# Performance work log

Measured on AMD Instinct MI355X. Metric: run time of the kernel, lower is better.

## Reference

```python
import jax, jax.numpy as jnp
import numpy as np
from jax import lax

B, T, F = 4096, 100, 40
H_ENC, H_LAT, H_DEC = 64, 32, 64


def _lstm(x, Wih, Whh, b):
    """PyTorch-convention LSTM (gate order i,f,g,o), batch_first, zero init state.
    x: [B,T,Fin], Wih: [4H,Fin], Whh: [4H,H], b: [4H] (= b_ih + b_hh).
    Returns hidden sequence [B,T,H]."""
    H = Whh.shape[1]
    # precompute input contributions for all timesteps in one GEMM
    xg = jnp.einsum('btf,gf->btg', x, Wih) + b  # [B,T,4H]
    h0 = jnp.zeros((x.shape[0], H), dtype=x.dtype)
    c0 = jnp.zeros((x.shape[0], H), dtype=x.dtype)

    def step(carry, gx_t):
        h, c = carry
        gates = gx_t + h @ Whh.T  # [B,4H]
        i, f, g, o = jnp.split(gates, 4, axis=-1)
        c = jax.nn.sigmoid(f) * c + jax.nn.sigmoid(i) * jnp.tanh(g)
        h = jax.nn.sigmoid(o) * jnp.tanh(c)
        return (h, c), h

    _, hs = lax.scan(step, (h0, c0), jnp.swapaxes(xg, 0, 1))  # [T,B,H]
    return jnp.swapaxes(hs, 0, 1)


def setup_inputs() -> dict:
    key = jax.random.key(0)
    ks = jax.random.split(key, 8)
    s = 0.05
    return {
        'x': jax.random.normal(ks[0], (B, T, F), dtype=jnp.float32),
        'enc_Wih': jax.random.normal(ks[1], (4 * H_ENC, F), dtype=jnp.float32) * s,
        'enc_Whh': jax.random.normal(ks[2], (4 * H_ENC, H_ENC), dtype=jnp.float32) * s,
        'enc_b': jnp.zeros((4 * H_ENC,), dtype=jnp.float32),
        'lat_Wih': jax.random.normal(ks[3], (4 * H_LAT, H_ENC), dtype=jnp.float32) * s,
        'lat_Whh': jax.random.normal(ks[4], (4 * H_LAT, H_LAT), dtype=jnp.float32) * s,
        'lat_b': jnp.zeros((4 * H_LAT,), dtype=jnp.float32),
        'dec_Wih': jax.random.normal(ks[5], (4 * H_DEC, H_LAT), dtype=jnp.float32) * s,
        'dec_Whh': jax.random.normal(ks[6], (4 * H_DEC, H_DEC), dtype=jnp.float32) * s,
        'dec_b': jnp.zeros((4 * H_DEC,), dtype=jnp.float32),
        'out_W': jax.random.normal(ks[7], (F, H_DEC), dtype=jnp.float32) * s,
        'out_b': jnp.zeros((F,), dtype=jnp.float32),
    }


def reference(x, enc_Wih, enc_Whh, enc_b, lat_Wih, lat_Whh, lat_b,
              dec_Wih, dec_Whh, dec_b, out_W, out_b):
    h = _lstm(x, enc_Wih, enc_Whh, enc_b)                 # [B,T,64]
    last = h[:, -1:, :]                                   # [B,1,64]
    rep = jnp.broadcast_to(last, (h.shape[0], h.shape[1], last.shape[-1]))
    h = _lstm(rep, lat_Wih, lat_Whh, lat_b)               # [B,T,32]
    h = _lstm(h, dec_Wih, dec_Whh, dec_b)                 # [B,T,64]
    return jnp.einsum('bth,fh->btf', h, out_W) + out_b    # [B,T,40]
```

## Files before the change

### kernel.cpp

```cpp
#include <hip/hip_runtime.h>
#include <cstddef>

typedef __attribute__((ext_vector_type(8))) short bf16x8;
typedef __attribute__((ext_vector_type(4))) float f32x4;

#define MFMA(a, b, c) __builtin_amdgcn_mfma_f32_16x16x32_bf16((a), (b), (c), 0, 0, 0)

static __device__ __forceinline__ unsigned short f2bf(float f) {
  unsigned u = __builtin_bit_cast(unsigned, f);
  u = u + 0x7FFFu + ((u >> 16) & 1u);
  return (unsigned short)(u >> 16);
}
static __device__ __forceinline__ float bf2f(unsigned short h) {
  unsigned u = ((unsigned)h) << 16;
  return __builtin_bit_cast(float, u);
}
static __device__ __forceinline__ float fast_sig(float x) {
  return __builtin_amdgcn_rcpf(1.0f + __expf(-x));
}
static __device__ __forceinline__ float fast_tanh(float x) {
  return 2.0f * __builtin_amdgcn_rcpf(1.0f + __expf(-2.0f * x)) - 1.0f;
}

static __device__ __forceinline__ void lds_barrier() {
  asm volatile("s_waitcnt lgkmcnt(0)\n\ts_barrier" ::: "memory");
}

static __device__ __forceinline__ bf16x8 aread(const char* base, int lane, int kc) {
  int b = lane & 15, g = lane >> 4;
  int off = (kc * 64 + g * 16) ^ ((b & 7) << 4);
  return *(const bf16x8*)(base + b * 256 + off);
}
static __device__ __forceinline__ void awrite16(char* base, int b, int k, unsigned short v) {
  int off = (2 * k) ^ ((b & 7) << 4);
  *(unsigned short*)(base + b * 256 + off) = v;
}
static __device__ __forceinline__ void awrite32(char* base, int b, int k, unsigned v) {
  int off = (2 * k) ^ ((b & 7) << 4);
  *(unsigned*)(base + b * 256 + off) = v;
}

extern "C" __global__ __launch_bounds__(512, 2)
void lstm_ae_mfma5(const float* __restrict__ x,
                   const float* __restrict__ eWih, const float* __restrict__ eWhh, const float* __restrict__ eb,
                   const float* __restrict__ lWih, const float* __restrict__ lWhh, const float* __restrict__ lb,
                   const float* __restrict__ dWih, const float* __restrict__ dWhh, const float* __restrict__ db,
                   const float* __restrict__ oW,  const float* __restrict__ ob,
                   float* __restrict__ out)
{
  __shared__ __align__(16) char sAhi[2][4096];
  __shared__ __align__(16) char sAlo[2][4096];

  const int tid  = threadIdx.x;
  const int lane = tid & 63;
  const int w    = tid >> 6;
  const int c16  = lane & 15;
  const int p4   = lane >> 4;
  const int bbase = blockIdx.x * 16;

  {
    f32x4 z = {0.f, 0.f, 0.f, 0.f};
    *(f32x4*)(&sAhi[0][0] + tid * 16) = z;
    *(f32x4*)(&sAlo[0][0] + tid * 16) = z;
  }

  bf16x8 ewh[2][4], ewl[2][4];
  float ebias[2][4];
#pragma unroll
  for (int n = 0; n < 2; ++n) {
    int tr = c16;
    int u = w * 8 + (tr >> 2) * 2 + n;
    int ga = tr & 3;
#pragma unroll
    for (int r = 0; r < 4; ++r) ebias[n][r] = eb[r * 64 + (w * 8 + p4 * 2 + n)];
#pragma unroll
    for (int kc = 0; kc < 4; ++kc) {
      bf16x8 hi, lo;
#pragma unroll
      for (int e = 0; e < 8; ++e) {
        int k = kc * 32 + p4 * 8 + e;
        float v = 0.f;
        if (k < 40)       v = eWih[(ga * 64 + u) * 40 + k];
        else if (k >= 64) v = eWhh[(ga * 64 + u) * 64 + (k - 64)];
        unsigned short hh = f2bf(v);
        hi[e] = (short)hh;
        lo[e] = (short)f2bf(v - bf2f(hh));
      }
      ewh[n][kc] = hi; ewl[n][kc] = lo;
    }
  }

  lds_barrier();

  const bool stager = (tid < 160);
  const int sb = tid / 10, sf4 = tid - (tid / 10) * 10;
  if (stager) {
    f32x4 ld = *(const f32x4*)(x + ((size_t)(bbase + sb) * 100 + 0) * 40 + sf4 * 4);
    unsigned long long ph = 0, pl = 0;
#pragma unroll
    for (int e = 0; e < 4; ++e) {
      unsigned short hh = f2bf(ld[e]);
      unsigned short ll = f2bf(ld[e] - bf2f(hh));
      ph |= (unsigned long long)hh << (16 * e);
      pl |= (unsigned long long)ll << (16 * e);
    }
    int off = (sf4 * 8) ^ ((sb & 7) << 4);
    *(unsigned long long*)(sAhi[0] + sb * 256 + off) = ph;
    *(unsigned long long*)(sAlo[0] + sb * 256 + off) = pl;
  }
  f32x4 xldA = {0.f, 0.f, 0.f, 0.f}, xldB = {0.f, 0.f, 0.f, 0.f};
  if (stager)
    xldA = *(const f32x4*)(x + ((size_t)(bbase + sb) * 100 + 1) * 40 + sf4 * 4);

  float cE[2] = {0.f, 0.f};
  lds_barrier();

  auto enc_step = [&](int t, const char* Rh, const char* Rl, char* Wh, char* Wl,
                      f32x4& xin, f32x4& xout) {
    if (stager) {
      unsigned long long ph = 0, pl = 0;
#pragma unroll
      for (int e = 0; e < 4; ++e) {
        unsigned short hh = f2bf(xin[e]);
        unsigned short ll = f2bf(xin[e] - bf2f(hh));
        ph |= (unsigned long long)hh << (16 * e);
        pl |= (unsigned long long)ll << (16 * e);
      }
      int off = (sf4 * 8) ^ ((sb & 7) << 4);
      *(unsigned long long*)(Wh + sb * 256 + off) = ph;
      *(unsigned long long*)(Wl + sb * 256 + off) = pl;
      int tn = (t + 2 <= 99) ? t + 2 : 99;
      xout = *(const f32x4*)(x + ((size_t)(bbase + sb) * 100 + tn) * 40 + sf4 * 4);
    }

    f32x4 acc[2], acc2[2];
#pragma unroll
    for (int n = 0; n < 2; ++n) {
      acc[n]  = f32x4{ebias[n][0], ebias[n][1], ebias[n][2], ebias[n][3]};
      acc2[n] = f32x4{0.f, 0.f, 0.f, 0.f};
    }
#pragma unroll
    for (int kc = 0; kc < 4; ++kc) {
      bf16x8 ah = aread(Rh, lane, kc);
      bf16x8 al = aread(Rl, lane, kc);
#pragma unroll
      for (int n = 0; n < 2; ++n) {
        f32x4 t0 = (kc < 2) ? acc[n] : acc2[n];
        t0 = MFMA(ewh[n][kc], ah, t0);
        t0 = MFMA(ewl[n][kc], ah, t0);
        t0 = MFMA(ewh[n][kc], al, t0);
        if (kc < 2) acc[n] = t0; else acc2[n] = t0;
      }
    }

    unsigned short hh[2], hl[2];
#pragma unroll
    for (int n = 0; n < 2; ++n) {
      f32x4 gv = acc[n] + acc2[n];
      float ii = fast_sig(gv[0]), ff = fast_sig(gv[1]);
      float gg = fast_tanh(gv[2]), oo = fast_sig(gv[3]);
      cE[n] = ff * cE[n] + ii * gg;
      float hv = oo * fast_tanh(cE[n]);
      hh[n] = f2bf(hv);
      hl[n] = f2bf(hv - bf2f(hh[n]));
    }
    awrite32(Wh, c16, 64 + w * 8 + p4 * 2, (unsigned)hh[0] | ((unsigned)hh[1] << 16));
    awrite32(Wl, c16, 64 + w * 8 + p4 * 2, (unsigned)hl[0] | ((unsigned)hl[1] << 16));

    lds_barrier();
  };

#pragma unroll 1
  for (int tt = 0; tt < 100; tt += 2) {
    enc_step(tt,     sAhi[0], sAlo[0], sAhi[1], sAlo[1], xldA, xldB);
    enc_step(tt + 1, sAhi[1], sAlo[1], sAhi[0], sAlo[0], xldB, xldA);
  }

  f32x4 xga;
  {
    int tr = c16;
    int u = w * 4 + (tr >> 2), ga = tr & 3;
    int ul = w * 4 + p4;
    xga = f32x4{lb[ul], lb[32 + ul], lb[64 + ul], lb[96 + ul]};
#pragma unroll
    for (int kci = 0; kci < 2; ++kci) {
      bf16x8 hi, lo;
#pragma unroll
      for (int e = 0; e < 8; ++e) {
        float v = lWih[(ga * 32 + u) * 64 + kci * 32 + p4 * 8 + e];
        unsigned short hh = f2bf(v);
        hi[e] = (short)hh;
        lo[e] = (short)f2bf(v - bf2f(hh));
      }
      bf16x8 ah = aread(sAhi[0], lane, 2 + kci);
      bf16x8 al = aread(sAlo[0], lane, 2 + kci);
      xga = MFMA(hi, ah, xga);
      xga = MFMA(lo, ah, xga);
      xga = MFMA(hi, al, xga);
    }
  }
  lds_barrier();

  {
    f32x4 z = {0.f, 0.f, 0.f, 0.f};
    *(f32x4*)(&sAhi[0][0] + tid * 16) = z;
    *(f32x4*)(&sAlo[0][0] + tid * 16) = z;
  }

  bf16x8 lwh, lwl;
  {
    int tr = c16;
    int u = w * 4 + (tr >> 2), ga = tr & 3;
    bf16x8 hi, lo;
#pragma unroll
    for (int e = 0; e < 8; ++e) {
      float v = lWhh[(ga * 32 + u) * 32 + p4 * 8 + e];
      unsigned short hh = f2bf(v);
      hi[e] = (short)hh;
      lo[e] = (short)f2bf(v - bf2f(hh));
    }
    lwh = hi; lwl = lo;
  }
  bf16x8 dwh[2][3], dwl[2][3];
  float dbias[2][4];
#pragma unroll
  for (int n = 0; n < 2; ++n) {
    int tr = c16;
    int u = w * 8 + (tr >> 2) * 2 + n;
    int ga = tr & 3;
#pragma unroll
    for (int r = 0; r < 4; ++r) dbias[n][r] = db[r * 64 + (w * 8 + p4 * 2 + n)];
#pragma unroll
    for (int kc = 0; kc < 3; ++kc) {
      bf16x8 hi, lo;
#pragma unroll
      for (int e = 0; e < 8; ++e) {
        int k = kc * 32 + p4 * 8 + e;
        float v = (k < 32) ? dWih[(ga * 64 + u) * 32 + k]
                           : dWhh[(ga * 64 + u) * 64 + (k - 32)];
        unsigned short hh = f2bf(v);
        hi[e] = (short)hh;
        lo[e] = (short)f2bf(v - bf2f(hh));
      }
      dwh[n][kc] = hi; dwl[n][kc] = lo;
    }
  }
  bf16x8 pwh[2], pwl[2];
  float pbias[4];
#pragma unroll
  for (int r = 0; r < 4; ++r) {
    int f = w * 16 + p4 * 4 + r;
    pbias[r] = (w < 3 && f < 40) ? ob[f] : 0.0f;
  }
  if (w < 3) {
    int f = w * 16 + c16;
#pragma unroll
    for (int kci = 0; kci < 2; ++kci) {
      bf16x8 hi, lo;
#pragma unroll
      for (int e = 0; e < 8; ++e) {
        float v = (f < 40) ? oW[f * 64 + kci * 32 + p4 * 8 + e] : 0.0f;
        unsigned short hh = f2bf(v);
        hi[e] = (short)hh;
        lo[e] = (short)f2bf(v - bf2f(hh));
      }
      pwh[kci] = hi; pwl[kci] = lo;
    }
  }

  float cL = 0.f;
  float cD[2] = {0.f, 0.f};
  lds_barrier();

#pragma unroll 1
  for (int i = 0; i < 102; ++i) {
    const int pa = i & 1;
    bf16x8 c0h = aread(sAhi[pa ^ 1], lane, 0), c0l = aread(sAlo[pa ^ 1], lane, 0);
    bf16x8 d1h = aread(sAhi[pa], lane, 1),     d1l = aread(sAlo[pa], lane, 1);
    bf16x8 d2h = aread(sAhi[pa], lane, 2),     d2l = aread(sAlo[pa], lane, 2);

    if (i < 100) {
      f32x4 lac = xga;
      lac = MFMA(lwh, c0h, lac);
      lac = MFMA(lwl, c0h, lac);
      lac = MFMA(lwh, c0l, lac);
      float ii = fast_sig(lac[0]), ff = fast_sig(lac[1]);
      float gg = fast_tanh(lac[2]), oo = fast_sig(lac[3]);
      cL = ff * cL + ii * gg;
      float hv = oo * fast_tanh(cL);
      unsigned short hhh = f2bf(hv);
      awrite16(sAhi[pa], c16, w * 4 + p4, hhh);
      awrite16(sAlo[pa], c16, w * 4 + p4, f2bf(hv - bf2f(hhh)));
    }

    if (i >= 1 && i < 101) {
      unsigned short hh[2], hl[2];
#pragma unroll
      for (int n = 0; n < 2; ++n) {
        f32x4 dac = f32x4{dbias[n][0], dbias[n][1], dbias[n][2], dbias[n][3]};
        dac = MFMA(dwh[n][0], c0h, dac);
        dac = MFMA(dwl[n][0], c0h, dac);
        dac = MFMA(dwh[n][0], c0l, dac);
        dac = MFMA(dwh[n][1], d1h, dac);
        dac = MFMA(dwl[n][1], d1h, dac);
        dac = MFMA(dwh[n][1], d1l, dac);
        dac = MFMA(dwh[n][2], d2h, dac);
        dac = MFMA(dwl[n][2], d2h, dac);
        dac = MFMA(dwh[n][2], d2l, dac);
        float ii = fast_sig(dac[0]), ff = fast_sig(dac[1]);
        float gg = fast_tanh(dac[2]), oo = fast_sig(dac[3]);
        cD[n] = ff * cD[n] + ii * gg;
        float hv = oo * fast_tanh(cD[n]);
        hh[n] = f2bf(hv);
        hl[n] = f2bf(hv - bf2f(hh[n]));
      }
      awrite32(sAhi[pa ^ 1], c16, 32 + w * 8 + p4 * 2, (unsigned)hh[0] | ((unsigned)hh[1] << 16));
      awrite32(sAlo[pa ^ 1], c16, 32 + w * 8 + p4 * 2, (unsigned)hl[0] | ((unsigned)hl[1] << 16));
    }

    if (i >= 2 && w < 3) {
      f32x4 pac = f32x4{pbias[0], pbias[1], pbias[2], pbias[3]};
      pac = MFMA(pwh[0], d1h, pac);
      pac = MFMA(pwl[0], d1h, pac);
      pac = MFMA(pwh[0], d1l, pac);
      pac = MFMA(pwh[1], d2h, pac);
      pac = MFMA(pwl[1], d2h, pac);
      pac = MFMA(pwh[1], d2l, pac);
#pragma unroll
      for (int r = 0; r < 4; ++r) {
        int f = w * 16 + p4 * 4 + r;
        if (f < 40)
          out[((size_t)(bbase + c16) * 100 + (i - 2)) * 40 + f] = pac[r];
      }
    }
    lds_barrier();
  }
}

extern "C" void kernel_launch(void* const* d_in, const int* in_sizes, int n_in,
                              void* d_out, int out_size, void* d_ws, size_t ws_size,
                              hipStream_t stream) {
  const float* x    = (const float*)d_in[0];
  const float* eWih = (const float*)d_in[1];
  const float* eWhh = (const float*)d_in[2];
  const float* eb   = (const float*)d_in[3];
  const float* lWih = (const float*)d_in[4];
  const float* lWhh = (const float*)d_in[5];
  const float* lb   = (const float*)d_in[6];
  const float* dWih = (const float*)d_in[7];
  const float* dWhh = (const float*)d_in[8];
  const float* db   = (const float*)d_in[9];
  const float* oW   = (const float*)d_in[10];
  const float* ob   = (const float*)d_in[11];
  float* out = (float*)d_out;

  lstm_ae_mfma5<<<256, 512, 0, stream>>>(x, eWih, eWhh, eb, lWih, lWhh, lb,
                                         dWih, dWhh, db, oW, ob, out);
}
```

Before: 184.1 us.

## Split LSTM work across 16 waves with producer/consumer encoder input projection

Doubles the block to 1024 threads. In the encoder, 8 waves compute the input projection for the next timestep and hand the partial gates to the other 8 waves through a new LDS buffer. Those 8 recurrent waves add only the hidden-state contribution, which shortens each wave's per-step MFMA chain. The decoder is re-split so each of 16 waves handles one gate unit column, the latent LSTM runs on 8 waves, and the output projection moves to waves 13-15. Occupancy drops to one block per CU and LDS use grows, in exchange for shorter serial dependency chains per step.

```diff
diff --git a/kernel.cpp b/kernel.cpp
--- a/kernel.cpp
+++ b/kernel.cpp
@@ -40,8 +40,8 @@
   *(unsigned*)(base + b * 256 + off) = v;
 }
 
-extern "C" __global__ __launch_bounds__(512, 2)
-void lstm_ae_mfma5(const float* __restrict__ x,
+extern "C" __global__ __launch_bounds__(1024, 1)
+void lstm_ae_mfma6(const float* __restrict__ x,
                    const float* __restrict__ eWih, const float* __restrict__ eWhh, const float* __restrict__ eb,
                    const float* __restrict__ lWih, const float* __restrict__ lWhh, const float* __restrict__ lb,
                    const float* __restrict__ dWih, const float* __restrict__ dWhh, const float* __restrict__ db,
@@ -50,6 +50,7 @@
 {
   __shared__ __align__(16) char sAhi[2][4096];
   __shared__ __align__(16) char sAlo[2][4096];
+  __shared__ __align__(16) char sP[2][16384];
 
   const int tid  = threadIdx.x;
   const int lane = tid & 63;
@@ -57,129 +58,145 @@
   const int c16  = lane & 15;
   const int p4   = lane >> 4;
   const int bbase = blockIdx.x * 16;
-
-  {
+  const bool xw = (w < 8);
+  const int p   = w & 7;
+
+  if (tid < 512) {
     f32x4 z = {0.f, 0.f, 0.f, 0.f};
     *(f32x4*)(&sAhi[0][0] + tid * 16) = z;
     *(f32x4*)(&sAlo[0][0] + tid * 16) = z;
   }
 
-  bf16x8 ewh[2][4], ewl[2][4];
+  bf16x8 wfh[2][2], wfl[2][2];
   float ebias[2][4];
 #pragma unroll
   for (int n = 0; n < 2; ++n) {
-    int tr = c16;
-    int u = w * 8 + (tr >> 2) * 2 + n;
-    int ga = tr & 3;
-#pragma unroll
-    for (int r = 0; r < 4; ++r) ebias[n][r] = eb[r * 64 + (w * 8 + p4 * 2 + n)];
-#pragma unroll
-    for (int kc = 0; kc < 4; ++kc) {
+    int u = p * 8 + (c16 >> 2) * 2 + n;
+    int ga = c16 & 3;
+    if (xw) {
+#pragma unroll
+      for (int r = 0; r < 4; ++r) ebias[n][r] = eb[r * 64 + (p * 8 + p4 * 2 + n)];
+    }
+#pragma unroll
+    for (int kci = 0; kci < 2; ++kci) {
       bf16x8 hi, lo;
 #pragma unroll
       for (int e = 0; e < 8; ++e) {
-        int k = kc * 32 + p4 * 8 + e;
-        float v = 0.f;
-        if (k < 40)       v = eWih[(ga * 64 + u) * 40 + k];
-        else if (k >= 64) v = eWhh[(ga * 64 + u) * 64 + (k - 64)];
+        int k = kci * 32 + p4 * 8 + e;
+        float v;
+        if (xw) v = (k < 40) ? eWih[(ga * 64 + u) * 40 + k] : 0.0f;
+        else    v = eWhh[(ga * 64 + u) * 64 + k];
         unsigned short hh = f2bf(v);
         hi[e] = (short)hh;
         lo[e] = (short)f2bf(v - bf2f(hh));
       }
-      ewh[n][kc] = hi; ewl[n][kc] = lo;
-    }
-  }
-
-  lds_barrier();
-
-  const bool stager = (tid < 160);
-  const int sb = tid / 10, sf4 = tid - (tid / 10) * 10;
-  if (stager) {
-    f32x4 ld = *(const f32x4*)(x + ((size_t)(bbase + sb) * 100 + 0) * 40 + sf4 * 4);
-    unsigned long long ph = 0, pl = 0;
-#pragma unroll
-    for (int e = 0; e < 4; ++e) {
-      unsigned short hh = f2bf(ld[e]);
-      unsigned short ll = f2bf(ld[e] - bf2f(hh));
-      ph |= (unsigned long long)hh << (16 * e);
-      pl |= (unsigned long long)ll << (16 * e);
-    }
-    int off = (sf4 * 8) ^ ((sb & 7) << 4);
-    *(unsigned long long*)(sAhi[0] + sb * 256 + off) = ph;
-    *(unsigned long long*)(sAlo[0] + sb * 256 + off) = pl;
-  }
-  f32x4 xldA = {0.f, 0.f, 0.f, 0.f}, xldB = {0.f, 0.f, 0.f, 0.f};
-  if (stager)
-    xldA = *(const f32x4*)(x + ((size_t)(bbase + sb) * 100 + 1) * 40 + sf4 * 4);
+      wfh[n][kci] = hi; wfl[n][kci] = lo;
+    }
+  }
+
+  lds_barrier();
+
+  const bool st = (tid < 320);
+  const int sbb = tid / 20, sf0 = (tid % 20) * 2;
+  if (st) {
+#pragma unroll
+    for (int tau = 0; tau < 2; ++tau) {
+      float2 v = *(const float2*)(x + ((size_t)(bbase + sbb) * 100 + tau) * 40 + sf0);
+      unsigned short h0 = f2bf(v.x), h1 = f2bf(v.y);
+      unsigned short l0 = f2bf(v.x - bf2f(h0)), l1 = f2bf(v.y - bf2f(h1));
+      awrite32(sAhi[tau], sbb, sf0, (unsigned)h0 | ((unsigned)h1 << 16));
+      awrite32(sAlo[tau], sbb, sf0, (unsigned)l0 | ((unsigned)l1 << 16));
+    }
+  }
+  float2 xin = {0.f, 0.f};
+  if (st) xin = *(const float2*)(x + ((size_t)(bbase + sbb) * 100 + 2) * 40 + sf0);
+  lds_barrier();
+
+  const int pswz  = (c16 & 7) << 4;
+  const int poff0 = (c16 * 1024 + (p * 32 + p4 * 4) * 4) ^ pswz;
+  const int poff1 = (c16 * 1024 + (p * 32 + 16 + p4 * 4) * 4) ^ pswz;
+
+  if (xw) {
+    bf16x8 x0h = aread(sAhi[0], lane, 0), x0l = aread(sAlo[0], lane, 0);
+    bf16x8 x1h = aread(sAhi[0], lane, 1), x1l = aread(sAlo[0], lane, 1);
+#pragma unroll
+    for (int n = 0; n < 2; ++n) {
+      f32x4 aA = f32x4{ebias[n][0], ebias[n][1], ebias[n][2], ebias[n][3]};
+      aA = MFMA(wfh[n][0], x0h, aA);
+      aA = MFMA(wfl[n][0], x0h, aA);
+      aA = MFMA(wfh[n][0], x0l, aA);
+      f32x4 aB = f32x4{0.f, 0.f, 0.f, 0.f};
+      aB = MFMA(wfh[n][1], x1h, aB);
+      aB = MFMA(wfl[n][1], x1h, aB);
+      aB = MFMA(wfh[n][1], x1l, aB);
+      f32x4 r = aA + aB;
+      *(f32x4*)(sP[0] + ((n == 0) ? poff0 : poff1)) = r;
+    }
+  }
+  lds_barrier();
 
   float cE[2] = {0.f, 0.f};
-  lds_barrier();
-
-  auto enc_step = [&](int t, const char* Rh, const char* Rl, char* Wh, char* Wl,
-                      f32x4& xin, f32x4& xout) {
-    if (stager) {
-      unsigned long long ph = 0, pl = 0;
-#pragma unroll
-      for (int e = 0; e < 4; ++e) {
-        unsigned short hh = f2bf(xin[e]);
-        unsigned short ll = f2bf(xin[e] - bf2f(hh));
-        ph |= (unsigned long long)hh << (16 * e);
-        pl |= (unsigned long long)ll << (16 * e);
-      }
-      int off = (sf4 * 8) ^ ((sb & 7) << 4);
-      *(unsigned long long*)(Wh + sb * 256 + off) = ph;
-      *(unsigned long long*)(Wl + sb * 256 + off) = pl;
-      int tn = (t + 2 <= 99) ? t + 2 : 99;
-      xout = *(const f32x4*)(x + ((size_t)(bbase + sb) * 100 + tn) * 40 + sf4 * 4);
-    }
-
-    f32x4 acc[2], acc2[2];
-#pragma unroll
-    for (int n = 0; n < 2; ++n) {
-      acc[n]  = f32x4{ebias[n][0], ebias[n][1], ebias[n][2], ebias[n][3]};
-      acc2[n] = f32x4{0.f, 0.f, 0.f, 0.f};
-    }
-#pragma unroll
-    for (int kc = 0; kc < 4; ++kc) {
-      bf16x8 ah = aread(Rh, lane, kc);
-      bf16x8 al = aread(Rl, lane, kc);
+
+#pragma unroll 1
+  for (int t = 0; t < 100; ++t) {
+    const int rb = (t + 1) & 1, wb = t & 1;
+    if (xw) {
+      bf16x8 x0h = aread(sAhi[rb], lane, 0), x0l = aread(sAlo[rb], lane, 0);
+      bf16x8 x1h = aread(sAhi[rb], lane, 1), x1l = aread(sAlo[rb], lane, 1);
 #pragma unroll
       for (int n = 0; n < 2; ++n) {
-        f32x4 t0 = (kc < 2) ? acc[n] : acc2[n];
-        t0 = MFMA(ewh[n][kc], ah, t0);
-        t0 = MFMA(ewl[n][kc], ah, t0);
-        t0 = MFMA(ewh[n][kc], al, t0);
-        if (kc < 2) acc[n] = t0; else acc2[n] = t0;
-      }
-    }
-
-    unsigned short hh[2], hl[2];
-#pragma unroll
-    for (int n = 0; n < 2; ++n) {
-      f32x4 gv = acc[n] + acc2[n];
-      float ii = fast_sig(gv[0]), ff = fast_sig(gv[1]);
-      float gg = fast_tanh(gv[2]), oo = fast_sig(gv[3]);
-      cE[n] = ff * cE[n] + ii * gg;
-      float hv = oo * fast_tanh(cE[n]);
-      hh[n] = f2bf(hv);
-      hl[n] = f2bf(hv - bf2f(hh[n]));
-    }
-    awrite32(Wh, c16, 64 + w * 8 + p4 * 2, (unsigned)hh[0] | ((unsigned)hh[1] << 16));
-    awrite32(Wl, c16, 64 + w * 8 + p4 * 2, (unsigned)hl[0] | ((unsigned)hl[1] << 16));
-
+        f32x4 aA = f32x4{ebias[n][0], ebias[n][1], ebias[n][2], ebias[n][3]};
+        aA = MFMA(wfh[n][0], x0h, aA);
+        aA = MFMA(wfl[n][0], x0h, aA);
+        aA = MFMA(wfh[n][0], x0l, aA);
+        f32x4 aB = f32x4{0.f, 0.f, 0.f, 0.f};
+        aB = MFMA(wfh[n][1], x1h, aB);
+        aB = MFMA(wfl[n][1], x1h, aB);
+        aB = MFMA(wfh[n][1], x1l, aB);
+        f32x4 r = aA + aB;
+        *(f32x4*)(sP[rb] + ((n == 0) ? poff0 : poff1)) = r;
+      }
+      if (st) {
+        unsigned short h0 = f2bf(xin.x), h1 = f2bf(xin.y);
+        unsigned short l0 = f2bf(xin.x - bf2f(h0)), l1 = f2bf(xin.y - bf2f(h1));
+        awrite32(sAhi[wb], sbb, sf0, (unsigned)h0 | ((unsigned)h1 << 16));
+        awrite32(sAlo[wb], sbb, sf0, (unsigned)l0 | ((unsigned)l1 << 16));
+        int tn = (t + 3 <= 99) ? t + 3 : 99;
+        xin = *(const float2*)(x + ((size_t)(bbase + sbb) * 100 + tn) * 40 + sf0);
+      }
+    } else {
+      f32x4 acc0 = *(const f32x4*)(sP[wb] + poff0);
+      f32x4 acc1 = *(const f32x4*)(sP[wb] + poff1);
+      bf16x8 h2h = aread(sAhi[rb], lane, 2), h2l = aread(sAlo[rb], lane, 2);
+      bf16x8 h3h = aread(sAhi[rb], lane, 3), h3l = aread(sAlo[rb], lane, 3);
+      unsigned short hh[2], hl[2];
+#pragma unroll
+      for (int n = 0; n < 2; ++n) {
+        f32x4 aA = (n == 0) ? acc0 : acc1;
+        aA = MFMA(wfh[n][0], h2h, aA);
+        aA = MFMA(wfl[n][0], h2h, aA);
+        aA = MFMA(wfh[n][0], h2l, aA);
+        f32x4 aB = f32x4{0.f, 0.f, 0.f, 0.f};
+        aB = MFMA(wfh[n][1], h3h, aB);
+        aB = MFMA(wfl[n][1], h3h, aB);
+        aB = MFMA(wfh[n][1], h3l, aB);
+        f32x4 gv = aA + aB;
+        float ii = fast_sig(gv[0]), ff = fast_sig(gv[1]);
+        float gg = fast_tanh(gv[2]), oo = fast_sig(gv[3]);
+        cE[n] = ff * cE[n] + ii * gg;
+        float hv = oo * fast_tanh(cE[n]);
+        hh[n] = f2bf(hv);
+        hl[n] = f2bf(hv - bf2f(hh[n]));
+      }
+      awrite32(sAhi[wb], c16, 64 + p * 8 + p4 * 2, (unsigned)hh[0] | ((unsigned)hh[1] << 16));
+      awrite32(sAlo[wb], c16, 64 + p * 8 + p4 * 2, (unsigned)hl[0] | ((unsigned)hl[1] << 16));
+    }
     lds_barrier();
-  };
-
-#pragma unroll 1
-  for (int tt = 0; tt < 100; tt += 2) {
-    enc_step(tt,     sAhi[0], sAlo[0], sAhi[1], sAlo[1], xldA, xldB);
-    enc_step(tt + 1, sAhi[1], sAlo[1], sAhi[0], sAlo[0], xldB, xldA);
-  }
-
-  f32x4 xga;
-  {
-    int tr = c16;
-    int u = w * 4 + (tr >> 2), ga = tr & 3;
+  }
+
+  f32x4 xga = {0.f, 0.f, 0.f, 0.f};
+  if (w < 8) {
+    int u = w * 4 + (c16 >> 2), ga = c16 & 3;
     int ul = w * 4 + p4;
     xga = f32x4{lb[ul], lb[32 + ul], lb[64 + ul], lb[96 + ul]};
 #pragma unroll
@@ -192,8 +209,8 @@
         hi[e] = (short)hh;
         lo[e] = (short)f2bf(v - bf2f(hh));
       }
-      bf16x8 ah = aread(sAhi[0], lane, 2 + kci);
-      bf16x8 al = aread(sAlo[0], lane, 2 + kci);
+      bf16x8 ah = aread(sAhi[1], lane, 2 + kci);
+      bf16x8 al = aread(sAlo[1], lane, 2 + kci);
       xga = MFMA(hi, ah, xga);
       xga = MFMA(lo, ah, xga);
       xga = MFMA(hi, al, xga);
@@ -201,35 +218,20 @@
   }
   lds_barrier();
 
-  {
+  if (tid < 512) {
     f32x4 z = {0.f, 0.f, 0.f, 0.f};
     *(f32x4*)(&sAhi[0][0] + tid * 16) = z;
     *(f32x4*)(&sAlo[0][0] + tid * 16) = z;
   }
 
-  bf16x8 lwh, lwl;
+  bf16x8 dwh[3], dwl[3];
+  float dbias[4];
   {
-    int tr = c16;
-    int u = w * 4 + (tr >> 2), ga = tr & 3;
-    bf16x8 hi, lo;
-#pragma unroll
-    for (int e = 0; e < 8; ++e) {
-      float v = lWhh[(ga * 32 + u) * 32 + p4 * 8 + e];
-      unsigned short hh = f2bf(v);
-      hi[e] = (short)hh;
-      lo[e] = (short)f2bf(v - bf2f(hh));
-    }
-    lwh = hi; lwl = lo;
-  }
-  bf16x8 dwh[2][3], dwl[2][3];
-  float dbias[2][4];
-#pragma unroll
-  for (int n = 0; n < 2; ++n) {
-    int tr = c16;
-    int u = w * 8 + (tr >> 2) * 2 + n;
-    int ga = tr & 3;
-#pragma unroll
-    for (int r = 0; r < 4; ++r) dbias[n][r] = db[r * 64 + (w * 8 + p4 * 2 + n)];
+    int u = (w >> 1) * 8 + (c16 >> 2) * 2 + (w & 1);
+    int ga = c16 & 3;
+    int un = (w >> 1) * 8 + p4 * 2 + (w & 1);
+#pragma unroll
+    for (int r = 0; r < 4; ++r) dbias[r] = db[r * 64 + un];
 #pragma unroll
     for (int kc = 0; kc < 3; ++kc) {
       bf16x8 hi, lo;
@@ -242,18 +244,32 @@
         hi[e] = (short)hh;
         lo[e] = (short)f2bf(v - bf2f(hh));
       }
-      dwh[n][kc] = hi; dwl[n][kc] = lo;
-    }
-  }
-  bf16x8 pwh[2], pwl[2];
+      dwh[kc] = hi; dwl[kc] = lo;
+    }
+  }
+  bf16x8 lwh = {}, lwl = {};
+  if (w < 8) {
+    int u = w * 4 + (c16 >> 2), ga = c16 & 3;
+    bf16x8 hi, lo;
+#pragma unroll
+    for (int e = 0; e < 8; ++e) {
+      float v = lWhh[(ga * 32 + u) * 32 + p4 * 8 + e];
+      unsigned short hh = f2bf(v);
+      hi[e] = (short)hh;
+      lo[e] = (short)f2bf(v - bf2f(hh));
+    }
+    lwh = hi; lwl = lo;
+  }
+  bf16x8 pwh[2] = {}, pwl[2] = {};
   float pbias[4];
+  const int wp = w - 13;
 #pragma unroll
   for (int r = 0; r < 4; ++r) {
-    int f = w * 16 + p4 * 4 + r;
-    pbias[r] = (w < 3 && f < 40) ? ob[f] : 0.0f;
-  }
-  if (w < 3) {
-    int f = w * 16 + c16;
+    int f = wp * 16 + p4 * 4 + r;
+    pbias[r] = (w >= 13 && f < 40) ? ob[f] : 0.0f;
+  }
+  if (w >= 13) {
+    int f = wp * 16 + c16;
 #pragma unroll
     for (int kci = 0; kci < 2; ++kci) {
       bf16x8 hi, lo;
@@ -268,8 +284,7 @@
     }
   }
 
-  float cL = 0.f;
-  float cD[2] = {0.f, 0.f};
+  float cL = 0.f, cD = 0.f;
   lds_barrier();
 
 #pragma unroll 1
@@ -279,7 +294,7 @@
     bf16x8 d1h = aread(sAhi[pa], lane, 1),     d1l = aread(sAlo[pa], lane, 1);
     bf16x8 d2h = aread(sAhi[pa], lane, 2),     d2l = aread(sAlo[pa], lane, 2);
 
-    if (i < 100) {
+    if (i < 100 && w < 8) {
       f32x4 lac = xga;
       lac = MFMA(lwh, c0h, lac);
       lac = MFMA(lwl, c0h, lac);
@@ -294,41 +309,42 @@
     }
 
     if (i >= 1 && i < 101) {
-      unsigned short hh[2], hl[2];
-#pragma unroll
-      for (int n = 0; n < 2; ++n) {
-        f32x4 dac = f32x4{dbias[n][0], dbias[n][1], dbias[n][2], dbias[n][3]};
-        dac = MFMA(dwh[n][0], c0h, dac);
-        dac = MFMA(dwl[n][0], c0h, dac);
-        dac = MFMA(dwh[n][0], c0l, dac);
-        dac = MFMA(dwh[n][1], d1h, dac);
-        dac = MFMA(dwl[n][1], d1h, dac);
-        dac = MFMA(dwh[n][1], d1l, dac);
-        dac = MFMA(dwh[n][2], d2h, dac);
-        dac = MFMA(dwl[n][2], d2h, dac);
-        dac = MFMA(dwh[n][2], d2l, dac);
-        float ii = fast_sig(dac[0]), ff = fast_sig(dac[1]);
-        float gg = fast_tanh(dac[2]), oo = fast_sig(dac[3]);
-        cD[n] = ff * cD[n] + ii * gg;
-        float hv = oo * fast_tanh(cD[n]);
-        hh[n] = f2bf(hv);
-        hl[n] = f2bf(hv - bf2f(hh[n]));
-      }
-      awrite32(sAhi[pa ^ 1], c16, 32 + w * 8 + p4 * 2, (unsigned)hh[0] | ((unsigned)hh[1] << 16));
-      awrite32(sAlo[pa ^ 1], c16, 32 + w * 8 + p4 * 2, (unsigned)hl[0] | ((unsigned)hl[1] << 16));
-    }
-
-    if (i >= 2 && w < 3) {
-      f32x4 pac = f32x4{pbias[0], pbias[1], pbias[2], pbias[3]};
-      pac = MFMA(pwh[0], d1h, pac);
-      pac = MFMA(pwl[0], d1h, pac);
-      pac = MFMA(pwh[0], d1l, pac);
-      pac = MFMA(pwh[1], d2h, pac);
-      pac = MFMA(pwl[1], d2h, pac);
-      pac = MFMA(pwh[1], d2l, pac);
+      f32x4 dA = f32x4{dbias[0], dbias[1], dbias[2], dbias[3]};
+      dA = MFMA(dwh[0], c0h, dA);
+      dA = MFMA(dwl[0], c0h, dA);
+      dA = MFMA(dwh[0], c0l, dA);
+      f32x4 dB = f32x4{0.f, 0.f, 0.f, 0.f};
+      dB = MFMA(dwh[1], d1h, dB);
+      dB = MFMA(dwl[1], d1h, dB);
+      dB = MFMA(dwh[1], d1l, dB);
+      f32x4 dC = f32x4{0.f, 0.f, 0.f, 0.f};
+      dC = MFMA(dwh[2], d2h, dC);
+      dC = MFMA(dwl[2], d2h, dC);
+      dC = MFMA(dwh[2], d2l, dC);
+      f32x4 gv = (dA + dB) + dC;
+      float ii = fast_sig(gv[0]), ff = fast_sig(gv[1]);
+      float gg = fast_tanh(gv[2]), oo = fast_sig(gv[3]);
+      cD = ff * cD + ii * gg;
+      float hv = oo * fast_tanh(cD);
+      unsigned short hhh = f2bf(hv);
+      int k = 32 + (w >> 1) * 8 + p4 * 2 + (w & 1);
+      awrite16(sAhi[pa ^ 1], c16, k, hhh);
+      awrite16(sAlo[pa ^ 1], c16, k, f2bf(hv - bf2f(hhh)));
+    }
+
+    if (i >= 2 && w >= 13) {
+      f32x4 pA = f32x4{pbias[0], pbias[1], pbias[2], pbias[3]};
+      pA = MFMA(pwh[0], d1h, pA);
+      pA = MFMA(pwl[0], d1h, pA);
+      pA = MFMA(pwh[0], d1l, pA);
+      f32x4 pB = f32x4{0.f, 0.f, 0.f, 0.f};
+      pB = MFMA(pwh[1], d2h, pB);
+      pB = MFMA(pwl[1], d2h, pB);
+      pB = MFMA(pwh[1], d2l, pB);
+      f32x4 pac = pA + pB;
 #pragma unroll
       for (int r = 0; r < 4; ++r) {
-        int f = w * 16 + p4 * 4 + r;
+        int f = wp * 16 + p4 * 4 + r;
         if (f < 40)
           out[((size_t)(bbase + c16) * 100 + (i - 2)) * 40 + f] = pac[r];
       }
@@ -354,6 +370,6 @@
   const float* ob   = (const float*)d_in[11];
   float* out = (float*)d_out;
 
-  lstm_ae_mfma5<<<256, 512, 0, stream>>>(x, eWih, eWhh, eb, lWih, lWhh, lb,
-                                         dWih, dWhh, db, oW, ob, out);
-}
+  lstm_ae_mfma6<<<256, 1024, 0, stream>>>(x, eWih, eWhh, eb, lWih, lWhh, lb,
+                                          dWih, dWhh, db, oW, ob, out);
+}
```

New measurement: 219.6 us. 1.19x slower.

## Switch split-bf16 MFMA to fp16 with scaled weight residual and single activation copy

Applied to the files above, without the earlier changes.

Replaces the three-term bf16 hi/lo emulation with fp16 MFMAs. Weights are split into an fp16 hi part and a residual scaled by 2048, while activations are stored as a single fp16 copy. This cuts the MFMA count per gate tile from three to two, halves LDS reads and writes for activations, and lets the lo products accumulate in independent chains. The encoder's two-step unrolled lambda with double-buffered x prefetch becomes a plain loop that loads one step ahead. The trade-off is accuracy: activations carry only fp16 precision, and fp16 has a narrower exponent range than bf16.

```diff
diff --git a/kernel.cpp b/kernel.cpp
--- a/kernel.cpp
+++ b/kernel.cpp
@@ -1,19 +1,25 @@
 #include <hip/hip_runtime.h>
 #include <cstddef>
 
-typedef __attribute__((ext_vector_type(8))) short bf16x8;
+typedef _Float16 f16x8 __attribute__((ext_vector_type(8)));
 typedef __attribute__((ext_vector_type(4))) float f32x4;
 
-#define MFMA(a, b, c) __builtin_amdgcn_mfma_f32_16x16x32_bf16((a), (b), (c), 0, 0, 0)
-
-static __device__ __forceinline__ unsigned short f2bf(float f) {
-  unsigned u = __builtin_bit_cast(unsigned, f);
-  u = u + 0x7FFFu + ((u >> 16) & 1u);
-  return (unsigned short)(u >> 16);
-}
-static __device__ __forceinline__ float bf2f(unsigned short h) {
-  unsigned u = ((unsigned)h) << 16;
-  return __builtin_bit_cast(float, u);
+#define MFMA(a, b, c) __builtin_amdgcn_mfma_f32_16x16x32_f16((a), (b), (c), 0, 0, 0)
+
+static constexpr float LO_SCALE = 2048.0f;
+static constexpr float LO_INV   = 1.0f / 2048.0f;
+
+static __device__ __forceinline__ unsigned f2h_bits(float f) {
+  _Float16 h = (_Float16)f;
+  return (unsigned)__builtin_bit_cast(unsigned short, h);
+}
+static __device__ __forceinline__ unsigned pack16(unsigned a, unsigned b) {
+  return __builtin_amdgcn_perm(b, a, 0x05040100u);
+}
+static __device__ __forceinline__ void wsplit(float v, _Float16& hi, _Float16& lo) {
+  _Float16 h = (_Float16)v;
+  hi = h;
+  lo = (_Float16)((v - (float)h) * LO_SCALE);
 }
 static __device__ __forceinline__ float fast_sig(float x) {
   return __builtin_amdgcn_rcpf(1.0f + __expf(-x));
@@ -26,10 +32,10 @@
   asm volatile("s_waitcnt lgkmcnt(0)\n\ts_barrier" ::: "memory");
 }
 
-static __device__ __forceinline__ bf16x8 aread(const char* base, int lane, int kc) {
+static __device__ __forceinline__ f16x8 aread(const char* base, int lane, int kc) {
   int b = lane & 15, g = lane >> 4;
   int off = (kc * 64 + g * 16) ^ ((b & 7) << 4);
-  return *(const bf16x8*)(base + b * 256 + off);
+  return *(const f16x8*)(base + b * 256 + off);
 }
 static __device__ __forceinline__ void awrite16(char* base, int b, int k, unsigned short v) {
   int off = (2 * k) ^ ((b & 7) << 4);
@@ -41,15 +47,14 @@
 }
 
 extern "C" __global__ __launch_bounds__(512, 2)
-void lstm_ae_mfma5(const float* __restrict__ x,
+void lstm_ae_mfma9(const float* __restrict__ x,
                    const float* __restrict__ eWih, const float* __restrict__ eWhh, const float* __restrict__ eb,
                    const float* __restrict__ lWih, const float* __restrict__ lWhh, const float* __restrict__ lb,
                    const float* __restrict__ dWih, const float* __restrict__ dWhh, const float* __restrict__ db,
                    const float* __restrict__ oW,  const float* __restrict__ ob,
                    float* __restrict__ out)
 {
-  __shared__ __align__(16) char sAhi[2][4096];
-  __shared__ __align__(16) char sAlo[2][4096];
+  __shared__ __align__(16) char sA[2][4096];
 
   const int tid  = threadIdx.x;
   const int lane = tid & 63;
@@ -60,31 +65,29 @@
 
   {
     f32x4 z = {0.f, 0.f, 0.f, 0.f};
-    *(f32x4*)(&sAhi[0][0] + tid * 16) = z;
-    *(f32x4*)(&sAlo[0][0] + tid * 16) = z;
-  }
-
-  bf16x8 ewh[2][4], ewl[2][4];
+    *(f32x4*)(&sA[0][0] + tid * 16) = z;
+  }
+
+  f16x8 ewh[2][4], ewl[2][4];
   float ebias[2][4];
 #pragma unroll
   for (int n = 0; n < 2; ++n) {
-    int tr = c16;
-    int u = w * 8 + (tr >> 2) * 2 + n;
-    int ga = tr & 3;
+    int u = w * 8 + (c16 >> 2) * 2 + n;
+    int ga = c16 & 3;
 #pragma unroll
     for (int r = 0; r < 4; ++r) ebias[n][r] = eb[r * 64 + (w * 8 + p4 * 2 + n)];
 #pragma unroll
     for (int kc = 0; kc < 4; ++kc) {
-      bf16x8 hi, lo;
+      f16x8 hi, lo;
 #pragma unroll
       for (int e = 0; e < 8; ++e) {
         int k = kc * 32 + p4 * 8 + e;
         float v = 0.f;
         if (k < 40)       v = eWih[(ga * 64 + u) * 40 + k];
         else if (k >= 64) v = eWhh[(ga * 64 + u) * 64 + (k - 64)];
-        unsigned short hh = f2bf(v);
-        hi[e] = (short)hh;
-        lo[e] = (short)f2bf(v - bf2f(hh));
+        _Float16 h, l;
+        wsplit(v, h, l);
+        hi[e] = h; lo[e] = l;
       }
       ewh[n][kc] = hi; ewl[n][kc] = lo;
     }
@@ -96,156 +99,132 @@
   const int sb = tid / 10, sf4 = tid - (tid / 10) * 10;
   if (stager) {
     f32x4 ld = *(const f32x4*)(x + ((size_t)(bbase + sb) * 100 + 0) * 40 + sf4 * 4);
-    unsigned long long ph = 0, pl = 0;
-#pragma unroll
-    for (int e = 0; e < 4; ++e) {
-      unsigned short hh = f2bf(ld[e]);
-      unsigned short ll = f2bf(ld[e] - bf2f(hh));
-      ph |= (unsigned long long)hh << (16 * e);
-      pl |= (unsigned long long)ll << (16 * e);
-    }
+    unsigned long long pv =
+        (unsigned long long)pack16(f2h_bits(ld[0]), f2h_bits(ld[1]))
+      | ((unsigned long long)pack16(f2h_bits(ld[2]), f2h_bits(ld[3])) << 32);
     int off = (sf4 * 8) ^ ((sb & 7) << 4);
-    *(unsigned long long*)(sAhi[0] + sb * 256 + off) = ph;
-    *(unsigned long long*)(sAlo[0] + sb * 256 + off) = pl;
-  }
-  f32x4 xldA = {0.f, 0.f, 0.f, 0.f}, xldB = {0.f, 0.f, 0.f, 0.f};
-  if (stager)
-    xldA = *(const f32x4*)(x + ((size_t)(bbase + sb) * 100 + 1) * 40 + sf4 * 4);
+    *(unsigned long long*)(sA[0] + sb * 256 + off) = pv;
+  }
 
   float cE[2] = {0.f, 0.f};
+  int q = 0;
   lds_barrier();
 
-  auto enc_step = [&](int t, const char* Rh, const char* Rl, char* Wh, char* Wl,
-                      f32x4& xin, f32x4& xout) {
+#pragma unroll 1
+  for (int t = 0; t < 100; ++t) {
+    f32x4 xld;
     if (stager) {
-      unsigned long long ph = 0, pl = 0;
-#pragma unroll
-      for (int e = 0; e < 4; ++e) {
-        unsigned short hh = f2bf(xin[e]);
-        unsigned short ll = f2bf(xin[e] - bf2f(hh));
-        ph |= (unsigned long long)hh << (16 * e);
-        pl |= (unsigned long long)ll << (16 * e);
-      }
-      int off = (sf4 * 8) ^ ((sb & 7) << 4);
-      *(unsigned long long*)(Wh + sb * 256 + off) = ph;
-      *(unsigned long long*)(Wl + sb * 256 + off) = pl;
-      int tn = (t + 2 <= 99) ? t + 2 : 99;
-      xout = *(const f32x4*)(x + ((size_t)(bbase + sb) * 100 + tn) * 40 + sf4 * 4);
-    }
-
-    f32x4 acc[2], acc2[2];
+      int tn = (t + 1 < 100) ? t + 1 : 99;
+      xld = *(const f32x4*)(x + ((size_t)(bbase + sb) * 100 + tn) * 40 + sf4 * 4);
+    }
+
+    f32x4 acc[2], accL[2];
 #pragma unroll
     for (int n = 0; n < 2; ++n) {
       acc[n]  = f32x4{ebias[n][0], ebias[n][1], ebias[n][2], ebias[n][3]};
-      acc2[n] = f32x4{0.f, 0.f, 0.f, 0.f};
-    }
+      accL[n] = f32x4{0.f, 0.f, 0.f, 0.f};
+    }
+    const char* A = sA[q];
 #pragma unroll
     for (int kc = 0; kc < 4; ++kc) {
-      bf16x8 ah = aread(Rh, lane, kc);
-      bf16x8 al = aread(Rl, lane, kc);
+      f16x8 a = aread(A, lane, kc);
 #pragma unroll
       for (int n = 0; n < 2; ++n) {
-        f32x4 t0 = (kc < 2) ? acc[n] : acc2[n];
-        t0 = MFMA(ewh[n][kc], ah, t0);
-        t0 = MFMA(ewl[n][kc], ah, t0);
-        t0 = MFMA(ewh[n][kc], al, t0);
-        if (kc < 2) acc[n] = t0; else acc2[n] = t0;
-      }
-    }
-
-    unsigned short hh[2], hl[2];
+        acc[n]  = MFMA(ewh[n][kc], a, acc[n]);
+        accL[n] = MFMA(ewl[n][kc], a, accL[n]);
+      }
+    }
+
+    char* AN = sA[q ^ 1];
+    unsigned hb[2];
 #pragma unroll
     for (int n = 0; n < 2; ++n) {
-      f32x4 gv = acc[n] + acc2[n];
+      f32x4 gv = acc[n] + accL[n] * LO_INV;
       float ii = fast_sig(gv[0]), ff = fast_sig(gv[1]);
       float gg = fast_tanh(gv[2]), oo = fast_sig(gv[3]);
       cE[n] = ff * cE[n] + ii * gg;
       float hv = oo * fast_tanh(cE[n]);
-      hh[n] = f2bf(hv);
-      hl[n] = f2bf(hv - bf2f(hh[n]));
-    }
-    awrite32(Wh, c16, 64 + w * 8 + p4 * 2, (unsigned)hh[0] | ((unsigned)hh[1] << 16));
-    awrite32(Wl, c16, 64 + w * 8 + p4 * 2, (unsigned)hl[0] | ((unsigned)hl[1] << 16));
-
+      hb[n] = f2h_bits(hv);
+    }
+    awrite32(AN, c16, 64 + w * 8 + p4 * 2, pack16(hb[0], hb[1]));
+
+    if (stager) {
+      unsigned long long pv =
+          (unsigned long long)pack16(f2h_bits(xld[0]), f2h_bits(xld[1]))
+        | ((unsigned long long)pack16(f2h_bits(xld[2]), f2h_bits(xld[3])) << 32);
+      int off = (sf4 * 8) ^ ((sb & 7) << 4);
+      *(unsigned long long*)(AN + sb * 256 + off) = pv;
+    }
     lds_barrier();
-  };
-
-#pragma unroll 1
-  for (int tt = 0; tt < 100; tt += 2) {
-    enc_step(tt,     sAhi[0], sAlo[0], sAhi[1], sAlo[1], xldA, xldB);
-    enc_step(tt + 1, sAhi[1], sAlo[1], sAhi[0], sAlo[0], xldB, xldA);
+    q ^= 1;
   }
 
   f32x4 xga;
   {
-    int tr = c16;
-    int u = w * 4 + (tr >> 2), ga = tr & 3;
+    int u = w * 4 + (c16 >> 2), ga = c16 & 3;
     int ul = w * 4 + p4;
     xga = f32x4{lb[ul], lb[32 + ul], lb[64 + ul], lb[96 + ul]};
+    f32x4 xgaL = {0.f, 0.f, 0.f, 0.f};
 #pragma unroll
     for (int kci = 0; kci < 2; ++kci) {
-      bf16x8 hi, lo;
+      f16x8 hi, lo;
 #pragma unroll
       for (int e = 0; e < 8; ++e) {
         float v = lWih[(ga * 32 + u) * 64 + kci * 32 + p4 * 8 + e];
-        unsigned short hh = f2bf(v);
-        hi[e] = (short)hh;
-        lo[e] = (short)f2bf(v - bf2f(hh));
-      }
-      bf16x8 ah = aread(sAhi[0], lane, 2 + kci);
-      bf16x8 al = aread(sAlo[0], lane, 2 + kci);
-      xga = MFMA(hi, ah, xga);
-      xga = MFMA(lo, ah, xga);
-      xga = MFMA(hi, al, xga);
-    }
+        _Float16 h, l;
+        wsplit(v, h, l);
+        hi[e] = h; lo[e] = l;
+      }
+      f16x8 a = aread(sA[q], lane, 2 + kci);
+      xga  = MFMA(hi, a, xga);
+      xgaL = MFMA(lo, a, xgaL);
+    }
+    xga = xga + xgaL * LO_INV;
   }
   lds_barrier();
 
   {
     f32x4 z = {0.f, 0.f, 0.f, 0.f};
-    *(f32x4*)(&sAhi[0][0] + tid * 16) = z;
-    *(f32x4*)(&sAlo[0][0] + tid * 16) = z;
-  }
-
-  bf16x8 lwh, lwl;
+    *(f32x4*)(&sA[0][0] + tid * 16) = z;
+  }
+
+  f16x8 lwh, lwl;
   {
-    int tr = c16;
-    int u = w * 4 + (tr >> 2), ga = tr & 3;
-    bf16x8 hi, lo;
+    int u = w * 4 + (c16 >> 2), ga = c16 & 3;
+    f16x8 hi, lo;
 #pragma unroll
     for (int e = 0; e < 8; ++e) {
       float v = lWhh[(ga * 32 + u) * 32 + p4 * 8 + e];
-      unsigned short hh = f2bf(v);
-      hi[e] = (short)hh;
-      lo[e] = (short)f2bf(v - bf2f(hh));
+      _Float16 h, l;
+      wsplit(v, h, l);
+      hi[e] = h; lo[e] = l;
     }
     lwh = hi; lwl = lo;
   }
-  bf16x8 dwh[2][3], dwl[2][3];
+  f16x8 dwh[2][3], dwl[2][3];
   float dbias[2][4];
 #pragma unroll
   for (int n = 0; n < 2; ++n) {
-    int tr = c16;
-    int u = w * 8 + (tr >> 2) * 2 + n;
-    int ga = tr & 3;
+    int u = w * 8 + (c16 >> 2) * 2 + n;
+    int ga = c16 & 3;
 #pragma unroll
     for (int r = 0; r < 4; ++r) dbias[n][r] = db[r * 64 + (w * 8 + p4 * 2 + n)];
 #pragma unroll
     for (int kc = 0; kc < 3; ++kc) {
-      bf16x8 hi, lo;
+      f16x8 hi, lo;
 #pragma unroll
       for (int e = 0; e < 8; ++e) {
         int k = kc * 32 + p4 * 8 + e;
         float v = (k < 32) ? dWih[(ga * 64 + u) * 32 + k]
                            : dWhh[(ga * 64 + u) * 64 + (k - 32)];
-        unsigned short hh = f2bf(v);
-        hi[e] = (short)hh;
-        lo[e] = (short)f2bf(v - bf2f(hh));
+        _Float16 h, l;
+        wsplit(v, h, l);
+        hi[e] = h; lo[e] = l;
       }
       dwh[n][kc] = hi; dwl[n][kc] = lo;
     }
   }
-  bf16x8 pwh[2], pwl[2];
+  f16x8 pwh[2], pwl[2];
   float pbias[4];
 #pragma unroll
   for (int r = 0; r < 4; ++r) {
@@ -256,13 +235,13 @@
     int f = w * 16 + c16;
 #pragma unroll
     for (int kci = 0; kci < 2; ++kci) {
-      bf16x8 hi, lo;
+      f16x8 hi, lo;
 #pragma unroll
       for (int e = 0; e < 8; ++e) {
         float v = (f < 40) ? oW[f * 64 + kci * 32 + p4 * 8 + e] : 0.0f;
-        unsigned short hh = f2bf(v);
-        hi[e] = (short)hh;
-        lo[e] = (short)f2bf(v - bf2f(hh));
+        _Float16 h, l;
+        wsplit(v, h, l);
+        hi[e] = h; lo[e] = l;
       }
       pwh[kci] = hi; pwl[kci] = lo;
     }
@@ -275,62 +254,57 @@
 #pragma unroll 1
   for (int i = 0; i < 102; ++i) {
     const int pa = i & 1;
-    bf16x8 c0h = aread(sAhi[pa ^ 1], lane, 0), c0l = aread(sAlo[pa ^ 1], lane, 0);
-    bf16x8 d1h = aread(sAhi[pa], lane, 1),     d1l = aread(sAlo[pa], lane, 1);
-    bf16x8 d2h = aread(sAhi[pa], lane, 2),     d2l = aread(sAlo[pa], lane, 2);
+    f16x8 c0 = aread(sA[pa ^ 1], lane, 0);
+    f16x8 d1 = aread(sA[pa], lane, 1);
+    f16x8 d2 = aread(sA[pa], lane, 2);
 
     if (i < 100) {
-      f32x4 lac = xga;
-      lac = MFMA(lwh, c0h, lac);
-      lac = MFMA(lwl, c0h, lac);
-      lac = MFMA(lwh, c0l, lac);
-      float ii = fast_sig(lac[0]), ff = fast_sig(lac[1]);
-      float gg = fast_tanh(lac[2]), oo = fast_sig(lac[3]);
+      f32x4 lac = xga, lacL = {0.f, 0.f, 0.f, 0.f};
+      lac  = MFMA(lwh, c0, lac);
+      lacL = MFMA(lwl, c0, lacL);
+      f32x4 gv = lac + lacL * LO_INV;
+      float ii = fast_sig(gv[0]), ff = fast_sig(gv[1]);
+      float gg = fast_tanh(gv[2]), oo = fast_sig(gv[3]);
       cL = ff * cL + ii * gg;
       float hv = oo * fast_tanh(cL);
-      unsigned short hhh = f2bf(hv);
-      awrite16(sAhi[pa], c16, w * 4 + p4, hhh);
-      awrite16(sAlo[pa], c16, w * 4 + p4, f2bf(hv - bf2f(hhh)));
+      awrite16(sA[pa], c16, w * 4 + p4, (unsigned short)f2h_bits(hv));
     }
 
     if (i >= 1 && i < 101) {
-      unsigned short hh[2], hl[2];
+      unsigned hb[2];
 #pragma unroll
       for (int n = 0; n < 2; ++n) {
         f32x4 dac = f32x4{dbias[n][0], dbias[n][1], dbias[n][2], dbias[n][3]};
-        dac = MFMA(dwh[n][0], c0h, dac);
-        dac = MFMA(dwl[n][0], c0h, dac);
-        dac = MFMA(dwh[n][0], c0l, dac);
-        dac = MFMA(dwh[n][1], d1h, dac);
-        dac = MFMA(dwl[n][1], d1h, dac);
-        dac = MFMA(dwh[n][1], d1l, dac);
-        dac = MFMA(dwh[n][2], d2h, dac);
-        dac = MFMA(dwl[n][2], d2h, dac);
-        dac = MFMA(dwh[n][2], d2l, dac);
-        float ii = fast_sig(dac[0]), ff = fast_sig(dac[1]);
-        float gg = fast_tanh(dac[2]), oo = fast_sig(dac[3]);
+        f32x4 dacL = {0.f, 0.f, 0.f, 0.f};
+        dac  = MFMA(dwh[n][0], c0, dac);
+        dacL = MFMA(dwl[n][0], c0, dacL);
+        dac  = MFMA(dwh[n][1], d1, dac);
+        dacL = MFMA(dwl[n][1], d1, dacL);
+        dac  = MFMA(dwh[n][2], d2, dac);
+        dacL = MFMA(dwl[n][2], d2, dacL);
+        f32x4 gv = dac + dacL * LO_INV;
+        float ii = fast_sig(gv[0]), ff = fast_sig(gv[1]);
+        float gg = fast_tanh(gv[2]), oo = fast_sig(gv[3]);
         cD[n] = ff * cD[n] + ii * gg;
         float hv = oo * fast_tanh(cD[n]);
-        hh[n] = f2bf(hv);
-        hl[n] = f2bf(hv - bf2f(hh[n]));
-      }
-      awrite32(sAhi[pa ^ 1], c16, 32 + w * 8 + p4 * 2, (unsigned)hh[0] | ((unsigned)hh[1] << 16));
-      awrite32(sAlo[pa ^ 1], c16, 32 + w * 8 + p4 * 2, (unsigned)hl[0] | ((unsigned)hl[1] << 16));
+        hb[n] = f2h_bits(hv);
+      }
+      awrite32(sA[pa ^ 1], c16, 32 + w * 8 + p4 * 2, pack16(hb[0], hb[1]));
     }
 
     if (i >= 2 && w < 3) {
       f32x4 pac = f32x4{pbias[0], pbias[1], pbias[2], pbias[3]};
-      pac = MFMA(pwh[0], d1h, pac);
-      pac = MFMA(pwl[0], d1h, pac);
-      pac = MFMA(pwh[0], d1l, pac);
-      pac = MFMA(pwh[1], d2h, pac);
-      pac = MFMA(pwl[1], d2h, pac);
-      pac = MFMA(pwh[1], d2l, pac);
+      f32x4 pacL = {0.f, 0.f, 0.f, 0.f};
+      pac  = MFMA(pwh[0], d1, pac);
+      pacL = MFMA(pwl[0], d1, pacL);
+      pac  = MFMA(pwh[1], d2, pac);
+      pacL = MFMA(pwl[1], d2, pacL);
+      f32x4 pv = pac + pacL * LO_INV;
 #pragma unroll
       for (int r = 0; r < 4; ++r) {
         int f = w * 16 + p4 * 4 + r;
         if (f < 40)
-          out[((size_t)(bbase + c16) * 100 + (i - 2)) * 40 + f] = pac[r];
+          out[((size_t)(bbase + c16) * 100 + (i - 2)) * 40 + f] = pv[r];
       }
     }
     lds_barrier();
@@ -354,6 +328,6 @@
   const float* ob   = (const float*)d_in[11];
   float* out = (float*)d_out;
 
-  lstm_ae_mfma5<<<256, 512, 0, stream>>>(x, eWih, eWhh, eb, lWih, lWhh, lb,
+  lstm_ae_mfma9<<<256, 512, 0, stream>>>(x, eWih, eWhh, eb, lWih, lWhh, lb,
                                          dWih, dWhh, db, oW, ob, out);
 }
```

New measurement: 159.0 us. 1.16x faster.
